# Performance work log

Hardware: AMD Instinct MI355X
Metric: run time of the kernel (lower is better)

The kernel has to match this reference:

```python
import jax, jax.numpy as jnp
import numpy as np
import math

NUM_HEADS = 8
DIM = 512
HEAD_DIM = DIM // NUM_HEADS
SCALE = HEAD_DIM ** -0.5
RP = 2            # remove_pad = kernel_size//2 * 2 for kernel_size=3
EPS_GN = 1e-5     # GroupNorm eps
EPS_L1 = 1e-12    # F.normalize eps


def _conv(x, w, b):
    # x: [B, Cin, H, W], w: [Cout, Cin, 3, 3] (OIHW), VALID padding, stride 1
    y = jax.lax.conv_general_dilated(x, w, (1, 1), 'VALID',
                                     dimension_numbers=('NCHW', 'OIHW', 'NCHW'))
    return y + b[None, :, None, None]


def _gn_per_channel(x, g, b):
    # GroupNorm with num_groups == num_channels: per-channel norm over (H, W)
    mu = x.mean(axis=(-2, -1), keepdims=True)
    var = x.var(axis=(-2, -1), keepdims=True)
    xn = (x - mu) * jax.lax.rsqrt(var + EPS_GN)
    return xn * g[None, :, None, None] + b[None, :, None, None]


def _ppe(rpe, c1w, c1b, g1w, g1b, c2w, c2b, g2w, g2b):
    # PeripheralPositionEncoding: rpe [side^2, side^2, 4*H] -> [1, H, N, N], N=(side-2*RP)^2
    nr, _, d = rpe.shape
    side = int(round(math.sqrt(nr)))
    s2 = side - 2 * RP
    x = rpe.reshape(side, side, side, side, d)          # i j k l d
    x = x[RP:side - RP, RP:side - RP]                   # trim i, j borders
    x = x.transpose(0, 1, 4, 2, 3).reshape(s2 * s2, d, side, side)  # (ij) d k l
    x = jax.nn.relu(_gn_per_channel(_conv(x, c1w, c1b), g1w, g1b))
    x = _gn_per_channel(_conv(x, c2w, c2b), g2w, g2b)   # [(ij), H, s2, s2]
    y = x.reshape(s2 * s2, NUM_HEADS, s2 * s2).transpose(1, 0, 2)[None]  # [1,H,N,N]
    return jax.nn.sigmoid(y)


def setup_inputs() -> dict:
    key = jax.random.key(0)
    ks = jax.random.split(key, 12)
    B, N = 8, 1024            # N = (36 - 4)^2
    side = 36
    cin = NUM_HEADS * 4       # 32
    inp = {
        'x': jax.random.normal(ks[0], (B, N, DIM), jnp.float32),
        'rpe_embed': jax.random.normal(ks[1], (side * side, side * side, cin), jnp.float32),
        'wqkv': jax.random.normal(ks[2], (3 * DIM, DIM), jnp.float32) * 0.02,
        'wproj': jax.random.normal(ks[3], (DIM, DIM), jnp.float32) * 0.02,
        'bproj': jnp.zeros((DIM,), jnp.float32),
        'c1w': jax.random.normal(ks[4], (cin, cin, 3, 3), jnp.float32) * 0.02,
        'c1b': jnp.zeros((cin,), jnp.float32),
        'g1w': jnp.ones((cin,), jnp.float32),
        'g1b': jnp.zeros((cin,), jnp.float32),
        'c2w': jax.random.normal(ks[5], (NUM_HEADS, cin, 3, 3), jnp.float32) * 0.02,
        'c2b': jnp.zeros((NUM_HEADS,), jnp.float32),
        'g2w': jnp.ones((NUM_HEADS,), jnp.float32),        # norm_init[1] = 1.0
        'g2b': jnp.zeros((NUM_HEADS,), jnp.float32),       # norm_init[0] = 0.0
    }
    return inp


def reference(x, rpe_embed, wqkv, wproj, bproj, c1w, c1b, g1w, g1b, c2w, c2b, g2w, g2b):
    B, N, D = x.shape
    H, HD = NUM_HEADS, HEAD_DIM
    qkv = x @ wqkv.T                                   # [B, N, 3D]
    q, k, v = jnp.split(qkv, 3, axis=-1)
    def heads(t):
        return t.reshape(B, N, H, HD).transpose(0, 2, 1, 3)  # [B, H, N, HD]
    q, k, v = heads(q), heads(k), heads(v)
    dots = jnp.einsum('bhnd,bhmd->bhnm', q, k) * SCALE
    dots = jnp.exp(dots - dots.max(axis=-1, keepdims=True))  # stable exp-score
    w = _ppe(rpe_embed, c1w, c1b, g1w, g1b, c2w, c2b, g2w, g2b)  # [1,H,N,N]
    attn = w * dots
    attn = attn / jnp.maximum(jnp.abs(attn).sum(axis=-1, keepdims=True), EPS_L1)  # L1 normalize
    out = jnp.einsum('bhnm,bhmd->bhnd', attn, v)
    out = out.transpose(0, 2, 1, 3).reshape(B, N, D)
    return out @ wproj.T + bproj
```

## Files before the change

### kernel.cpp

```cpp
#include <hip/hip_runtime.h>
#include <hip/hip_fp16.h>


typedef __attribute__((ext_vector_type(8))) short bf16x8;
typedef __attribute__((ext_vector_type(8))) _Float16 f16x8;
typedef __attribute__((ext_vector_type(4))) float f32x4;

__device__ __forceinline__ unsigned short f2bf(float f) {
  unsigned u = __builtin_bit_cast(unsigned, f);
  u += 0x7FFFu + ((u >> 16) & 1u);
  return (unsigned short)(u >> 16);
}

template<bool OUT_BF16>
__global__ __launch_bounds__(256) void gemm_f16_bt(
    const float* __restrict__ A, const float* __restrict__ B,
    void* __restrict__ Cv, const float* __restrict__ bias,
    int M, int N, int K)
{
  __shared__ __align__(16) _Float16 As[128 * 40];
  __shared__ __align__(16) _Float16 Bs[128 * 40];
  const int tid = threadIdx.x;
  const int wv = tid >> 6, ln = tid & 63, lr = ln & 15, lq = ln >> 4;
  const int wm = wv >> 1, wn = wv & 1;
  const int m0 = blockIdx.y * 128, n0 = blockIdx.x * 128;

  f32x4 acc[4][4];
#pragma unroll
  for (int i = 0; i < 4; i++)
#pragma unroll
    for (int j = 0; j < 4; j++) acc[i][j] = (f32x4){0.f, 0.f, 0.f, 0.f};

  const int sr = tid >> 1, sk = (tid & 1) * 16;
  const float* Ap = A + (size_t)(m0 + sr) * K + sk;
  const float* Bp = B + (size_t)(n0 + sr) * K + sk;

  for (int k0 = 0; k0 < K; k0 += 32) {
    float4 av0 = *(const float4*)(Ap + k0);
    float4 av1 = *(const float4*)(Ap + k0 + 4);
    float4 av2 = *(const float4*)(Ap + k0 + 8);
    float4 av3 = *(const float4*)(Ap + k0 + 12);
    float4 bv0 = *(const float4*)(Bp + k0);
    float4 bv1 = *(const float4*)(Bp + k0 + 4);
    float4 bv2 = *(const float4*)(Bp + k0 + 8);
    float4 bv3 = *(const float4*)(Bp + k0 + 12);
    __syncthreads();
    {
      f16x8 p0, p1, r0, r1;
      p0[0]=(_Float16)av0.x; p0[1]=(_Float16)av0.y; p0[2]=(_Float16)av0.z; p0[3]=(_Float16)av0.w;
      p0[4]=(_Float16)av1.x; p0[5]=(_Float16)av1.y; p0[6]=(_Float16)av1.z; p0[7]=(_Float16)av1.w;
      p1[0]=(_Float16)av2.x; p1[1]=(_Float16)av2.y; p1[2]=(_Float16)av2.z; p1[3]=(_Float16)av2.w;
      p1[4]=(_Float16)av3.x; p1[5]=(_Float16)av3.y; p1[6]=(_Float16)av3.z; p1[7]=(_Float16)av3.w;
      r0[0]=(_Float16)bv0.x; r0[1]=(_Float16)bv0.y; r0[2]=(_Float16)bv0.z; r0[3]=(_Float16)bv0.w;
      r0[4]=(_Float16)bv1.x; r0[5]=(_Float16)bv1.y; r0[6]=(_Float16)bv1.z; r0[7]=(_Float16)bv1.w;
      r1[0]=(_Float16)bv2.x; r1[1]=(_Float16)bv2.y; r1[2]=(_Float16)bv2.z; r1[3]=(_Float16)bv2.w;
      r1[4]=(_Float16)bv3.x; r1[5]=(_Float16)bv3.y; r1[6]=(_Float16)bv3.z; r1[7]=(_Float16)bv3.w;
      *(f16x8*)&As[sr * 40 + sk] = p0;
      *(f16x8*)&As[sr * 40 + sk + 8] = p1;
      *(f16x8*)&Bs[sr * 40 + sk] = r0;
      *(f16x8*)&Bs[sr * 40 + sk + 8] = r1;
    }
    __syncthreads();
    f16x8 af[4], bf[4];
#pragma unroll
    for (int mf = 0; mf < 4; mf++)
      af[mf] = *(const f16x8*)&As[(wm * 64 + mf * 16 + lr) * 40 + lq * 8];
#pragma unroll
    for (int nf = 0; nf < 4; nf++)
      bf[nf] = *(const f16x8*)&Bs[(wn * 64 + nf * 16 + lr) * 40 + lq * 8];
#pragma unroll
    for (int mf = 0; mf < 4; mf++)
#pragma unroll
      for (int nf = 0; nf < 4; nf++)
        acc[mf][nf] = __builtin_amdgcn_mfma_f32_16x16x32_f16(af[mf], bf[nf], acc[mf][nf], 0, 0, 0);
  }

#pragma unroll
  for (int mf = 0; mf < 4; mf++)
#pragma unroll
    for (int reg = 0; reg < 4; reg++) {
      const int row = m0 + wm * 64 + mf * 16 + lq * 4 + reg;
#pragma unroll
      for (int nf = 0; nf < 4; nf++) {
        const int col = n0 + wn * 64 + nf * 16 + lr;
        float v = acc[mf][nf][reg];
        if (bias) v += bias[col];
        if (OUT_BF16) ((unsigned short*)Cv)[(size_t)row * N + col] = f2bf(v);
        else          ((float*)Cv)[(size_t)row * N + col] = v;
      }
    }
}

__global__ __launch_bounds__(1024, 1) void conv_fused(
    const float* __restrict__ rpe,
    const float* __restrict__ c1w, const float* __restrict__ g1, const float* __restrict__ b1,
    const float* __restrict__ c2w, const float* __restrict__ g2, const float* __restrict__ b2,
    float* __restrict__ wout)
{
  extern __shared__ __align__(16) char smem[];
  unsigned short* inA = (unsigned short*)smem;
  unsigned short* yB  = (unsigned short*)(smem + 82944);
  unsigned short* wH1 = yB;
  unsigned short* wH2 = (unsigned short*)(smem + 156928);
  float* statA = (float*)(smem + 162688);
  float* aL    = (float*)(smem + 162944);
  float* cL    = aL + 32;
  float* transF = (float*)smem;

  const int tid = threadIdx.x;
  const int wv = tid >> 6, ln = tid & 63;
  const int lr = ln & 15, lq = ln >> 4;
  const int p = blockIdx.x;

  if (tid < 64) statA[tid] = 0.f;

  const float* src = rpe + (size_t)(((p >> 5) + 2) * 36 + (p & 31) + 2) * 41472;
  for (int t = tid; t < 10368; t += 1024) {
    int pix = t >> 3, dq = (t & 7) << 2;
    float4 v = *(const float4*)(src + pix * 32 + dq);
    __half2 h0 = __floats2half2_rn(v.x, v.y);
    __half2 h1 = __floats2half2_rn(v.z, v.w);
    uint2 u; u.x = __builtin_bit_cast(unsigned, h0); u.y = __builtin_bit_cast(unsigned, h1);
    *(uint2*)&inA[(dq >> 3) * 10368 + pix * 8 + (dq & 7)] = u;
  }
  for (int t = tid; t < 9216; t += 1024) {
    int oc = t / 288, rem = t - oc * 288;
    int ic = rem / 9, tap = rem - ic * 9;
    wH1[(tap * 32 + (oc & 1) * 16 + (oc >> 1)) * 40 + ic] = __half_as_ushort(__float2half(c1w[t]));
  }
  for (int t = tid; t < 2304; t += 1024) {
    int oc = t / 288, rem = t - oc * 288;
    int ic = rem / 9, tap = rem - ic * 9;
    wH2[(tap * 8 + oc) * 40 + ic] = __half_as_ushort(__float2half(c2w[t]));
  }
  __syncthreads();

  f16x8 w1f[2][9];
  const int ic0 = lq * 8;
#pragma unroll
  for (int ct = 0; ct < 2; ct++)
#pragma unroll
    for (int tap = 0; tap < 9; tap++)
      w1f[ct][tap] = *(const f16x8*)&wH1[(tap * 32 + ct * 16 + lr) * 40 + ic0];
  __syncthreads();

  constexpr int OFF1[9] = {0, 8, 16, 288, 296, 304, 576, 584, 592};
  float s0 = 0.f, q0 = 0.f, s1 = 0.f, q1 = 0.f;
  const unsigned short* inAg = inA + lq * 10368;
  for (int t = wv; t < 73; t += 16) {
    int m = t * 16 + lr;
    int ms = m < 1155 ? m : 1155;
    const unsigned short* ab = inAg + ((ms / 34) * 36 + (ms % 34)) * 8;
    f32x4 c0 = {0.f, 0.f, 0.f, 0.f}, c1v = {0.f, 0.f, 0.f, 0.f};
#pragma unroll
    for (int tap = 0; tap < 9; tap++) {
      f16x8 av = *(const f16x8*)(ab + OFF1[tap]);
      c0  = __builtin_amdgcn_mfma_f32_16x16x32_f16(av, w1f[0][tap], c0, 0, 0, 0);
      c1v = __builtin_amdgcn_mfma_f32_16x16x32_f16(av, w1f[1][tap], c1v, 0, 0, 0);
    }
#pragma unroll
    for (int r = 0; r < 4; r++) {
      int mo = t * 16 + lq * 4 + r;
      if (mo < 1156) {
        float v0 = c0[r], v1 = c1v[r];
        unsigned u = (unsigned)__half_as_ushort(__float2half(v0))
                   | ((unsigned)__half_as_ushort(__float2half(v1)) << 16);
        *(unsigned*)&yB[(lr >> 2) * 9248 + mo * 8 + ((lr * 2) & 7)] = u;
        s0 += v0; q0 += v0 * v0; s1 += v1; q1 += v1 * v1;
      }
    }
  }
#pragma unroll
  for (int off = 16; off < 64; off <<= 1) {
    s0 += __shfl_xor(s0, off); q0 += __shfl_xor(q0, off);
    s1 += __shfl_xor(s1, off); q1 += __shfl_xor(q1, off);
  }
  if (ln < 16) {
    atomicAdd(&statA[ln], s0);      atomicAdd(&statA[16 + ln], q0);
    atomicAdd(&statA[32 + ln], s1); atomicAdd(&statA[48 + ln], q1);
  }
  __syncthreads();
  if (tid < 32) {
    int cti = tid >> 4, lri = tid & 15;
    float s = statA[cti * 32 + lri];
    float q = statA[cti * 32 + 16 + lri];
    int ch = 2 * lri + cti;
    float mu = s * (1.f / 1156.f);
    float var = q * (1.f / 1156.f) - mu * mu;
    float a_ = rsqrtf(var + 1e-5f) * g1[ch];
    aL[ch] = a_; cL[ch] = b1[ch] - mu * a_;
  }
  if (tid < 16) statA[tid] = 0.f;
  __syncthreads();

  {
    int g = tid >> 8, ocb = g * 8;
    unsigned short* yg = yB + g * 9248;
    for (int pix = (tid & 255); pix < 1156; pix += 256) {
      f16x8 raw = *(const f16x8*)&yg[pix * 8];
      f16x8 outv;
#pragma unroll
      for (int e = 0; e < 8; e++) {
        float v = (float)raw[e];
        v = fmaxf(v * aL[ocb + e] + cL[ocb + e], 0.f);
        outv[e] = (_Float16)v;
      }
      *(f16x8*)&yg[pix * 8] = outv;
    }
  }
  __syncthreads();

  f16x8 w2f[9];
#pragma unroll
  for (int tap = 0; tap < 9; tap++)
    w2f[tap] = *(const f16x8*)&wH2[(tap * 8 + (lr & 7)) * 40 + ic0];

  constexpr int OFF2[9] = {0, 8, 16, 272, 280, 288, 544, 552, 560};
  const unsigned short* yBg = yB + lq * 9248;
  float s2 = 0.f, q2 = 0.f;
  for (int t = wv; t < 64; t += 16) {
    int m = t * 16 + lr;
    const unsigned short* ab = yBg + ((m >> 5) * 34 + (m & 31)) * 8;
    f32x4 cc = {0.f, 0.f, 0.f, 0.f};
#pragma unroll
    for (int tap = 0; tap < 9; tap++) {
      f16x8 av = *(const f16x8*)(ab + OFF2[tap]);
      cc = __builtin_amdgcn_mfma_f32_16x16x32_f16(av, w2f[tap], cc, 0, 0, 0);
    }
#pragma unroll
    for (int r = 0; r < 4; r++) {
      int mo = t * 16 + lq * 4 + r;
      float v = cc[r];
      if (lr < 8) {
        s2 += v; q2 += v * v;
        transF[lr * 1032 + mo] = v;
      }
    }
  }
#pragma unroll
  for (int off = 16; off < 64; off <<= 1) {
    s2 += __shfl_xor(s2, off); q2 += __shfl_xor(q2, off);
  }
  if (ln < 8) { atomicAdd(&statA[ln], s2); atomicAdd(&statA[8 + ln], q2); }
  __syncthreads();
  if (tid < 8) {
    float s = statA[tid], q = statA[8 + tid];
    float mu = s * (1.f / 1024.f);
    float var = q * (1.f / 1024.f) - mu * mu;
    float a_ = rsqrtf(var + 1e-5f) * g2[tid];
    aL[tid] = a_; cL[tid] = b2[tid] - mu * a_;
  }
  __syncthreads();

  for (int idx = tid; idx < 2048; idx += 1024) {
    int oc = idx >> 8, p4 = (idx & 255) << 2;
    float4 v = *(const float4*)&transF[oc * 1032 + p4];
    float a_ = aL[oc], c_ = cL[oc];
    float4 o;
    o.x = 1.f / (1.f + __expf(-(v.x * a_ + c_)));
    o.y = 1.f / (1.f + __expf(-(v.y * a_ + c_)));
    o.z = 1.f / (1.f + __expf(-(v.z * a_ + c_)));
    o.w = 1.f / (1.f + __expf(-(v.w * a_ + c_)));
    *(float4*)(wout + ((size_t)oc << 20) + ((size_t)p << 10) + p4) = o;
  }
}

__global__ __launch_bounds__(256) void attn_kernel(
    const unsigned short* __restrict__ qkv,
    const float* __restrict__ wppe,
    float* __restrict__ oh)
{
  __shared__ __align__(16) unsigned short k_lds[64 * 72];
  __shared__ __align__(16) unsigned short v_lds[64 * 72];
  __shared__ __align__(16) unsigned short p_lds[4 * 16 * 72];
  const int tid = threadIdx.x;
  const int wv = tid >> 6, ln = tid & 63;
  const int lr = ln & 15, lq = ln >> 4;
  const int b = blockIdx.y >> 3, h = blockIdx.y & 7;
  const int n0 = blockIdx.x << 6;

  const size_t qoff = (size_t)((b << 10) + n0 + (wv << 4) + lr) * 1536 + (h << 6);
  bf16x8 qf0 = *(const bf16x8*)(qkv + qoff + lq * 8);
  bf16x8 qf1 = *(const bf16x8*)(qkv + qoff + 32 + lq * 8);

  f32x4 acc[4];
#pragma unroll
  for (int dt = 0; dt < 4; dt++) acc[dt] = (f32x4){0.f, 0.f, 0.f, 0.f};
  float den[4] = {0.f, 0.f, 0.f, 0.f};
  const float* wp = wppe + ((size_t)h << 20);

  for (int m0 = 0; m0 < 1024; m0 += 64) {
    __syncthreads();
    for (int t = tid; t < 512; t += 256) {
      int m = t >> 3, dq = t & 7;
      const unsigned short* kr = qkv + (size_t)((b << 10) + m0 + m) * 1536 + 512 + (h << 6) + dq * 8;
      *(uint4*)&k_lds[m * 72 + dq * 8] = *(const uint4*)kr;
      uint4 vvv = *(const uint4*)(kr + 512);
      unsigned short tmp[8];
      *(uint4*)tmp = vvv;
#pragma unroll
      for (int i = 0; i < 8; i++) {
        int d = dq * 8 + i;
        v_lds[d * 72 + (m ^ (((d >> 3) & 7) << 3))] = tmp[i];
      }
    }
    __syncthreads();

    f32x4 s[4];
#pragma unroll
    for (int mt = 0; mt < 4; mt++) {
      const unsigned short* kb = &k_lds[(mt * 16 + lr) * 72 + lq * 8];
      f32x4 cz = (f32x4){0.f, 0.f, 0.f, 0.f};
      cz = __builtin_amdgcn_mfma_f32_16x16x32_bf16(qf0, *(const bf16x8*)kb, cz, 0, 0, 0);
      cz = __builtin_amdgcn_mfma_f32_16x16x32_bf16(qf1, *(const bf16x8*)(kb + 32), cz, 0, 0, 0);
      s[mt] = cz;
    }
#pragma unroll
    for (int mt = 0; mt < 4; mt++)
#pragma unroll
      for (int reg = 0; reg < 4; reg++) {
        int rrow = lq * 4 + reg;
        float wvl = wp[(size_t)(n0 + (wv << 4) + rrow) * 1024 + (m0 + mt * 16 + lr)];
        float pv = wvl * __expf(s[mt][reg] * 0.125f);
        den[reg] += pv;
        p_lds[((wv << 4) + rrow) * 72 + mt * 16 + lr] = f2bf(pv);
      }
    const unsigned short* pb = &p_lds[((wv << 4) + lr) * 72];
    bf16x8 pa0 = *(const bf16x8*)(pb + lq * 8);
    bf16x8 pa1 = *(const bf16x8*)(pb + 32 + lq * 8);
#pragma unroll
    for (int dt = 0; dt < 4; dt++) {
      int d = dt * 16 + lr;
      int sw = ((d >> 3) & 7) << 3;
      const unsigned short* vb = &v_lds[d * 72];
      acc[dt] = __builtin_amdgcn_mfma_f32_16x16x32_bf16(pa0, *(const bf16x8*)(vb + ((lq * 8) ^ sw)), acc[dt], 0, 0, 0);
      acc[dt] = __builtin_amdgcn_mfma_f32_16x16x32_bf16(pa1, *(const bf16x8*)(vb + ((32 + lq * 8) ^ sw)), acc[dt], 0, 0, 0);
    }
  }
#pragma unroll
  for (int off = 1; off < 16; off <<= 1)
#pragma unroll
    for (int reg = 0; reg < 4; reg++) den[reg] += __shfl_xor(den[reg], off);
#pragma unroll
  for (int dt = 0; dt < 4; dt++)
#pragma unroll
    for (int reg = 0; reg < 4; reg++) {
      size_t row = (size_t)((b << 10) + n0 + (wv << 4) + lq * 4 + reg);
      oh[row * 512 + (h << 6) + dt * 16 + lr] = acc[dt][reg] / den[reg];
    }
}

extern "C" void kernel_launch(void* const* d_in, const int* in_sizes, int n_in,
                              void* d_out, int out_size, void* d_ws, size_t ws_size,
                              hipStream_t stream) {
  (void)in_sizes; (void)n_in; (void)out_size; (void)ws_size;
  const float* x     = (const float*)d_in[0];
  const float* rpe   = (const float*)d_in[1];
  const float* wqkv  = (const float*)d_in[2];
  const float* wproj = (const float*)d_in[3];
  const float* bproj = (const float*)d_in[4];
  const float* c1w   = (const float*)d_in[5];
  const float* g1w   = (const float*)d_in[7];
  const float* g1b   = (const float*)d_in[8];
  const float* c2w   = (const float*)d_in[9];
  const float* g2w   = (const float*)d_in[11];
  const float* g2b   = (const float*)d_in[12];
  float* out = (float*)d_out;

  char* ws = (char*)d_ws;
  unsigned short* qkv_bf = (unsigned short*)ws;
  float* wppe = (float*)(ws + 25165824);
  float* ohb  = (float*)(ws + 58720256);

  gemm_f16_bt<true><<<dim3(12, 64), 256, 0, stream>>>(x, wqkv, qkv_bf, nullptr, 8192, 1536, 512);

  const int ldsC = 163200;
  hipFuncSetAttribute(reinterpret_cast<const void*>(&conv_fused),
                      hipFuncAttributeMaxDynamicSharedMemorySize, ldsC);
  conv_fused<<<1024, 1024, ldsC, stream>>>(rpe, c1w, g1w, g1b, c2w, g2w, g2b, wppe);

  attn_kernel<<<dim3(16, 64), 256, 0, stream>>>(qkv_bf, wppe, ohb);

  gemm_f16_bt<false><<<dim3(4, 64), 256, 0, stream>>>(ohb, wproj, out, bproj, 8192, 512, 512);
}
```

Baseline: 209.2 us.

## Split fused conv into two kernels with smaller LDS for higher occupancy

Replaces the single 1024-thread conv kernel, which used about 163KB of LDS and so fit one block per CU, with two kernels. conv1_k computes conv1 on half-images in 512-thread blocks with about 67KB of LDS and writes fp16 intermediates to global workspace. conv2_k reloads them, computes the GroupNorm statistics in a separate pass, then runs conv2 with its results kept in registers. The aim is more concurrent blocks per CU, so latency is hidden better, at the cost of an extra global round-trip for the intermediate and an additional launch. The y1g buffer reuses the ohb workspace region, which is safe because the writes are stream-ordered.

```diff
diff --git a/kernel.cpp b/kernel.cpp
--- a/kernel.cpp
+++ b/kernel.cpp
@@ -91,19 +91,81 @@
     }
 }
 
-__global__ __launch_bounds__(1024, 1) void conv_fused(
-    const float* __restrict__ rpe,
-    const float* __restrict__ c1w, const float* __restrict__ g1, const float* __restrict__ b1,
-    const float* __restrict__ c2w, const float* __restrict__ g2, const float* __restrict__ b2,
+__global__ __launch_bounds__(512, 4) void conv1_k(
+    const float* __restrict__ rpe, const float* __restrict__ c1w,
+    unsigned short* __restrict__ y1g)
+{
+  extern __shared__ __align__(16) char smem[];
+  unsigned short* inH = (unsigned short*)smem;
+  unsigned short* wH1 = (unsigned short*)(smem + 43776);
+
+  const int tid = threadIdx.x;
+  const int wv = tid >> 6, ln = tid & 63;
+  const int lr = ln & 15, lq = ln >> 4;
+  const int img = blockIdx.x >> 1, h = blockIdx.x & 1;
+
+  const float* src = rpe + (size_t)(((img >> 5) + 2) * 36 + (img & 31) + 2) * 41472
+                   + h * 19584;
+  for (int t = tid; t < 5472; t += 512) {
+    int pix = t >> 3, dq = (t & 7) << 2;
+    float4 v = *(const float4*)(src + t * 4);
+    __half2 h0 = __floats2half2_rn(v.x, v.y);
+    __half2 h1 = __floats2half2_rn(v.z, v.w);
+    uint2 u; u.x = __builtin_bit_cast(unsigned, h0); u.y = __builtin_bit_cast(unsigned, h1);
+    *(uint2*)&inH[(dq >> 3) * 5472 + pix * 8 + (dq & 7)] = u;
+  }
+  for (int t = tid; t < 9216; t += 512) {
+    int oc = t / 288, rem = t - oc * 288;
+    int ic = rem / 9, tap = rem - ic * 9;
+    wH1[(tap * 32 + (oc & 1) * 16 + (oc >> 1)) * 40 + ic] = __half_as_ushort(__float2half(c1w[t]));
+  }
+  __syncthreads();
+
+  const int ic0 = lq * 8;
+  f16x8 w1f[2][9];
+#pragma unroll
+  for (int ct = 0; ct < 2; ct++)
+#pragma unroll
+    for (int tap = 0; tap < 9; tap++)
+      w1f[ct][tap] = *(const f16x8*)&wH1[(tap * 32 + ct * 16 + lr) * 40 + ic0];
+
+  constexpr int OFF1[9] = {0, 8, 16, 288, 296, 304, 576, 584, 592};
+  unsigned short* ybase = y1g + (size_t)img * 36992 + (lr >> 2) * 9248 + ((2 * lr) & 7);
+  const unsigned short* inAg = inH + lq * 5472;
+  for (int t = wv; t < 37; t += 8) {
+    int m = t * 16 + lr;
+    int ms = m < 577 ? m : 577;
+    const unsigned short* ab = inAg + ((ms / 34) * 36 + (ms % 34)) * 8;
+    f32x4 c0 = {0.f, 0.f, 0.f, 0.f}, c1v = {0.f, 0.f, 0.f, 0.f};
+#pragma unroll
+    for (int tap = 0; tap < 9; tap++) {
+      f16x8 av = *(const f16x8*)(ab + OFF1[tap]);
+      c0  = __builtin_amdgcn_mfma_f32_16x16x32_f16(av, w1f[0][tap], c0, 0, 0, 0);
+      c1v = __builtin_amdgcn_mfma_f32_16x16x32_f16(av, w1f[1][tap], c1v, 0, 0, 0);
+    }
+#pragma unroll
+    for (int r = 0; r < 4; r++) {
+      int mo = t * 16 + lq * 4 + r;
+      if (mo < 578) {
+        unsigned u = (unsigned)__half_as_ushort(__float2half(c0[r]))
+                   | ((unsigned)__half_as_ushort(__float2half(c1v[r])) << 16);
+        *(unsigned*)(ybase + (h * 578 + mo) * 8) = u;
+      }
+    }
+  }
+}
+
+__global__ __launch_bounds__(512, 4) void conv2_k(
+    const unsigned short* __restrict__ y1g, const float* __restrict__ c2w,
+    const float* __restrict__ g1, const float* __restrict__ b1,
+    const float* __restrict__ g2, const float* __restrict__ b2,
     float* __restrict__ wout)
 {
   extern __shared__ __align__(16) char smem[];
-  unsigned short* inA = (unsigned short*)smem;
-  unsigned short* yB  = (unsigned short*)(smem + 82944);
-  unsigned short* wH1 = yB;
-  unsigned short* wH2 = (unsigned short*)(smem + 156928);
-  float* statA = (float*)(smem + 162688);
-  float* aL    = (float*)(smem + 162944);
+  unsigned short* yB  = (unsigned short*)smem;
+  unsigned short* wH2 = (unsigned short*)(smem + 73984);
+  float* statA = (float*)(smem + 79744);
+  float* aL    = statA + 64;
   float* cL    = aL + 32;
   float* transF = (float*)smem;
 
@@ -114,111 +176,85 @@
 
   if (tid < 64) statA[tid] = 0.f;
 
-  const float* src = rpe + (size_t)(((p >> 5) + 2) * 36 + (p & 31) + 2) * 41472;
-  for (int t = tid; t < 10368; t += 1024) {
-    int pix = t >> 3, dq = (t & 7) << 2;
-    float4 v = *(const float4*)(src + pix * 32 + dq);
-    __half2 h0 = __floats2half2_rn(v.x, v.y);
-    __half2 h1 = __floats2half2_rn(v.z, v.w);
-    uint2 u; u.x = __builtin_bit_cast(unsigned, h0); u.y = __builtin_bit_cast(unsigned, h1);
-    *(uint2*)&inA[(dq >> 3) * 10368 + pix * 8 + (dq & 7)] = u;
-  }
-  for (int t = tid; t < 9216; t += 1024) {
-    int oc = t / 288, rem = t - oc * 288;
-    int ic = rem / 9, tap = rem - ic * 9;
-    wH1[(tap * 32 + (oc & 1) * 16 + (oc >> 1)) * 40 + ic] = __half_as_ushort(__float2half(c1w[t]));
-  }
-  for (int t = tid; t < 2304; t += 1024) {
+  const unsigned short* src = y1g + (size_t)p * 36992;
+  for (int t = tid; t < 4624; t += 512)
+    *(uint4*)&yB[t * 8] = *(const uint4*)(src + t * 8);
+  for (int t = tid; t < 2304; t += 512) {
     int oc = t / 288, rem = t - oc * 288;
     int ic = rem / 9, tap = rem - ic * 9;
     wH2[(tap * 8 + oc) * 40 + ic] = __half_as_ushort(__float2half(c2w[t]));
   }
   __syncthreads();
 
-  f16x8 w1f[2][9];
-  const int ic0 = lq * 8;
-#pragma unroll
-  for (int ct = 0; ct < 2; ct++)
-#pragma unroll
-    for (int tap = 0; tap < 9; tap++)
-      w1f[ct][tap] = *(const f16x8*)&wH1[(tap * 32 + ct * 16 + lr) * 40 + ic0];
-  __syncthreads();
-
-  constexpr int OFF1[9] = {0, 8, 16, 288, 296, 304, 576, 584, 592};
-  float s0 = 0.f, q0 = 0.f, s1 = 0.f, q1 = 0.f;
-  const unsigned short* inAg = inA + lq * 10368;
-  for (int t = wv; t < 73; t += 16) {
-    int m = t * 16 + lr;
-    int ms = m < 1155 ? m : 1155;
-    const unsigned short* ab = inAg + ((ms / 34) * 36 + (ms % 34)) * 8;
-    f32x4 c0 = {0.f, 0.f, 0.f, 0.f}, c1v = {0.f, 0.f, 0.f, 0.f};
-#pragma unroll
-    for (int tap = 0; tap < 9; tap++) {
-      f16x8 av = *(const f16x8*)(ab + OFF1[tap]);
-      c0  = __builtin_amdgcn_mfma_f32_16x16x32_f16(av, w1f[0][tap], c0, 0, 0, 0);
-      c1v = __builtin_amdgcn_mfma_f32_16x16x32_f16(av, w1f[1][tap], c1v, 0, 0, 0);
-    }
-#pragma unroll
-    for (int r = 0; r < 4; r++) {
-      int mo = t * 16 + lq * 4 + r;
-      if (mo < 1156) {
-        float v0 = c0[r], v1 = c1v[r];
-        unsigned u = (unsigned)__half_as_ushort(__float2half(v0))
-                   | ((unsigned)__half_as_ushort(__float2half(v1)) << 16);
-        *(unsigned*)&yB[(lr >> 2) * 9248 + mo * 8 + ((lr * 2) & 7)] = u;
-        s0 += v0; q0 += v0 * v0; s1 += v1; q1 += v1 * v1;
-      }
-    }
-  }
-#pragma unroll
-  for (int off = 16; off < 64; off <<= 1) {
-    s0 += __shfl_xor(s0, off); q0 += __shfl_xor(q0, off);
-    s1 += __shfl_xor(s1, off); q1 += __shfl_xor(q1, off);
-  }
-  if (ln < 16) {
-    atomicAdd(&statA[ln], s0);      atomicAdd(&statA[16 + ln], q0);
-    atomicAdd(&statA[32 + ln], s1); atomicAdd(&statA[48 + ln], q1);
+  {
+    int g = wv >> 1;
+    float s[8], q[8];
+#pragma unroll
+    for (int e = 0; e < 8; e++) { s[e] = 0.f; q[e] = 0.f; }
+    int base = (wv & 1) * 64 + ln;
+    for (int k = 0; k < 10; k++) {
+      int pix = base + 128 * k;
+      if (pix < 1156) {
+        f16x8 v = *(const f16x8*)&yB[g * 9248 + pix * 8];
+#pragma unroll
+        for (int e = 0; e < 8; e++) { float f = (float)v[e]; s[e] += f; q[e] += f * f; }
+      }
+    }
+#pragma unroll
+    for (int off = 1; off < 64; off <<= 1)
+#pragma unroll
+      for (int e = 0; e < 8; e++) { s[e] += __shfl_xor(s[e], off); q[e] += __shfl_xor(q[e], off); }
+    if (ln == 0) {
+#pragma unroll
+      for (int e = 0; e < 8; e++) {
+        atomicAdd(&statA[g * 8 + e], s[e]);
+        atomicAdd(&statA[32 + g * 8 + e], q[e]);
+      }
+    }
   }
   __syncthreads();
   if (tid < 32) {
-    int cti = tid >> 4, lri = tid & 15;
-    float s = statA[cti * 32 + lri];
-    float q = statA[cti * 32 + 16 + lri];
-    int ch = 2 * lri + cti;
+    float s = statA[tid], q = statA[32 + tid];
     float mu = s * (1.f / 1156.f);
     float var = q * (1.f / 1156.f) - mu * mu;
-    float a_ = rsqrtf(var + 1e-5f) * g1[ch];
-    aL[ch] = a_; cL[ch] = b1[ch] - mu * a_;
+    float a_ = rsqrtf(var + 1e-5f) * g1[tid];
+    aL[tid] = a_; cL[tid] = b1[tid] - mu * a_;
   }
   if (tid < 16) statA[tid] = 0.f;
   __syncthreads();
 
   {
-    int g = tid >> 8, ocb = g * 8;
+    int g = tid >> 7, base = tid & 127;
     unsigned short* yg = yB + g * 9248;
-    for (int pix = (tid & 255); pix < 1156; pix += 256) {
-      f16x8 raw = *(const f16x8*)&yg[pix * 8];
-      f16x8 outv;
-#pragma unroll
-      for (int e = 0; e < 8; e++) {
-        float v = (float)raw[e];
-        v = fmaxf(v * aL[ocb + e] + cL[ocb + e], 0.f);
-        outv[e] = (_Float16)v;
-      }
-      *(f16x8*)&yg[pix * 8] = outv;
+    for (int k = 0; k < 10; k++) {
+      int pix = base + 128 * k;
+      if (pix < 1156) {
+        f16x8 raw = *(const f16x8*)&yg[pix * 8];
+        f16x8 outv;
+#pragma unroll
+        for (int e = 0; e < 8; e++) {
+          float v = (float)raw[e];
+          outv[e] = (_Float16)fmaxf(v * aL[g * 8 + e] + cL[g * 8 + e], 0.f);
+        }
+        *(f16x8*)&yg[pix * 8] = outv;
+      }
     }
   }
   __syncthreads();
 
   f16x8 w2f[9];
+  const int ic0 = lq * 8;
 #pragma unroll
   for (int tap = 0; tap < 9; tap++)
     w2f[tap] = *(const f16x8*)&wH2[(tap * 8 + (lr & 7)) * 40 + ic0];
 
   constexpr int OFF2[9] = {0, 8, 16, 272, 280, 288, 544, 552, 560};
   const unsigned short* yBg = yB + lq * 9248;
+  f32x4 zsave[8];
   float s2 = 0.f, q2 = 0.f;
-  for (int t = wv; t < 64; t += 16) {
+#pragma unroll
+  for (int i = 0; i < 8; i++) {
+    int t = wv + i * 8;
     int m = t * 16 + lr;
     const unsigned short* ab = yBg + ((m >> 5) * 34 + (m & 31)) * 8;
     f32x4 cc = {0.f, 0.f, 0.f, 0.f};
@@ -227,15 +263,9 @@
       f16x8 av = *(const f16x8*)(ab + OFF2[tap]);
       cc = __builtin_amdgcn_mfma_f32_16x16x32_f16(av, w2f[tap], cc, 0, 0, 0);
     }
-#pragma unroll
-    for (int r = 0; r < 4; r++) {
-      int mo = t * 16 + lq * 4 + r;
-      float v = cc[r];
-      if (lr < 8) {
-        s2 += v; q2 += v * v;
-        transF[lr * 1032 + mo] = v;
-      }
-    }
+    zsave[i] = cc;
+#pragma unroll
+    for (int r = 0; r < 4; r++) { s2 += cc[r]; q2 += cc[r] * cc[r]; }
   }
 #pragma unroll
   for (int off = 16; off < 64; off <<= 1) {
@@ -243,6 +273,16 @@
   }
   if (ln < 8) { atomicAdd(&statA[ln], s2); atomicAdd(&statA[8 + ln], q2); }
   __syncthreads();
+
+  if (lr < 8) {
+#pragma unroll
+    for (int i = 0; i < 8; i++) {
+      int t = wv + i * 8;
+#pragma unroll
+      for (int r = 0; r < 4; r++)
+        transF[lr * 1032 + t * 16 + lq * 4 + r] = zsave[i][r];
+    }
+  }
   if (tid < 8) {
     float s = statA[tid], q = statA[8 + tid];
     float mu = s * (1.f / 1024.f);
@@ -252,7 +292,7 @@
   }
   __syncthreads();
 
-  for (int idx = tid; idx < 2048; idx += 1024) {
+  for (int idx = tid; idx < 2048; idx += 512) {
     int oc = idx >> 8, p4 = (idx & 255) << 2;
     float4 v = *(const float4*)&transF[oc * 1032 + p4];
     float a_ = aL[oc], c_ = cL[oc];
@@ -370,14 +410,20 @@
   char* ws = (char*)d_ws;
   unsigned short* qkv_bf = (unsigned short*)ws;
   float* wppe = (float*)(ws + 25165824);
+  unsigned short* y1g = (unsigned short*)(ws + 58720256);
   float* ohb  = (float*)(ws + 58720256);
 
   gemm_f16_bt<true><<<dim3(12, 64), 256, 0, stream>>>(x, wqkv, qkv_bf, nullptr, 8192, 1536, 512);
 
-  const int ldsC = 163200;
-  hipFuncSetAttribute(reinterpret_cast<const void*>(&conv_fused),
-                      hipFuncAttributeMaxDynamicSharedMemorySize, ldsC);
-  conv_fused<<<1024, 1024, ldsC, stream>>>(rpe, c1w, g1w, g1b, c2w, g2w, g2b, wppe);
+  const int lds1 = 66816;
+  hipFuncSetAttribute(reinterpret_cast<const void*>(&conv1_k),
+                      hipFuncAttributeMaxDynamicSharedMemorySize, lds1);
+  conv1_k<<<2048, 512, lds1, stream>>>(rpe, c1w, y1g);
+
+  const int lds2 = 80256;
+  hipFuncSetAttribute(reinterpret_cast<const void*>(&conv2_k),
+                      hipFuncAttributeMaxDynamicSharedMemorySize, lds2);
+  conv2_k<<<1024, 512, lds2, stream>>>(y1g, c2w, g1w, g1b, g2w, g2b, wppe);
 
   attn_kernel<<<dim3(16, 64), 256, 0, stream>>>(qkv_bf, wppe, ohb);
 
```

Result: slower. 236.9 us (+13.2%).

## Read conv input directly from global and halve LDS to fit two blocks per CU

Applied to the files above, without the earlier changes.

The fused PPE conv kernel stops staging the full fp32 rpe patch into LDS as fp16. Instead each wave loads its conv1 input taps straight from global memory and converts them in registers. This cuts LDS use roughly in half and shrinks blocks to 512 threads, so more blocks can be resident per CU to overlap memory latency. Conv2 results are kept in registers until after the stats barrier so the transpose buffer can alias the conv1 output buffer. The cost is redundant global/L2 reads of overlapping 3x3 taps and higher register pressure.

```diff
diff --git a/kernel.cpp b/kernel.cpp
--- a/kernel.cpp
+++ b/kernel.cpp
@@ -91,20 +91,19 @@
     }
 }
 
-__global__ __launch_bounds__(1024, 1) void conv_fused(
+__global__ __launch_bounds__(512, 4) void conv_fused2(
     const float* __restrict__ rpe,
     const float* __restrict__ c1w, const float* __restrict__ g1, const float* __restrict__ b1,
     const float* __restrict__ c2w, const float* __restrict__ g2, const float* __restrict__ b2,
     float* __restrict__ wout)
 {
   extern __shared__ __align__(16) char smem[];
-  unsigned short* inA = (unsigned short*)smem;
-  unsigned short* yB  = (unsigned short*)(smem + 82944);
+  unsigned short* yB  = (unsigned short*)smem;
   unsigned short* wH1 = yB;
-  unsigned short* wH2 = (unsigned short*)(smem + 156928);
-  float* statA = (float*)(smem + 162688);
-  float* aL    = (float*)(smem + 162944);
-  float* cL    = aL + 32;
+  unsigned short* wH2 = (unsigned short*)(smem + 73984);
+  float* statA = (float*)(smem + 79744);
+  float* aL    = (float*)(smem + 80000);
+  float* cL    = (float*)(smem + 80128);
   float* transF = (float*)smem;
 
   const int tid = threadIdx.x;
@@ -114,21 +113,12 @@
 
   if (tid < 64) statA[tid] = 0.f;
 
-  const float* src = rpe + (size_t)(((p >> 5) + 2) * 36 + (p & 31) + 2) * 41472;
-  for (int t = tid; t < 10368; t += 1024) {
-    int pix = t >> 3, dq = (t & 7) << 2;
-    float4 v = *(const float4*)(src + pix * 32 + dq);
-    __half2 h0 = __floats2half2_rn(v.x, v.y);
-    __half2 h1 = __floats2half2_rn(v.z, v.w);
-    uint2 u; u.x = __builtin_bit_cast(unsigned, h0); u.y = __builtin_bit_cast(unsigned, h1);
-    *(uint2*)&inA[(dq >> 3) * 10368 + pix * 8 + (dq & 7)] = u;
-  }
-  for (int t = tid; t < 9216; t += 1024) {
+  for (int t = tid; t < 9216; t += 512) {
     int oc = t / 288, rem = t - oc * 288;
     int ic = rem / 9, tap = rem - ic * 9;
     wH1[(tap * 32 + (oc & 1) * 16 + (oc >> 1)) * 40 + ic] = __half_as_ushort(__float2half(c1w[t]));
   }
-  for (int t = tid; t < 2304; t += 1024) {
+  for (int t = tid; t < 2304; t += 512) {
     int oc = t / 288, rem = t - oc * 288;
     int ic = rem / 9, tap = rem - ic * 9;
     wH2[(tap * 8 + oc) * 40 + ic] = __half_as_ushort(__float2half(c2w[t]));
@@ -144,17 +134,21 @@
       w1f[ct][tap] = *(const f16x8*)&wH1[(tap * 32 + ct * 16 + lr) * 40 + ic0];
   __syncthreads();
 
-  constexpr int OFF1[9] = {0, 8, 16, 288, 296, 304, 576, 584, 592};
+  const float* src = rpe + (size_t)(((p >> 5) + 2) * 36 + (p & 31) + 2) * 41472;
+  constexpr int TOFF[9] = {0, 32, 64, 1152, 1184, 1216, 2304, 2336, 2368};
   float s0 = 0.f, q0 = 0.f, s1 = 0.f, q1 = 0.f;
-  const unsigned short* inAg = inA + lq * 10368;
-  for (int t = wv; t < 73; t += 16) {
+  for (int t = wv; t < 73; t += 8) {
     int m = t * 16 + lr;
     int ms = m < 1155 ? m : 1155;
-    const unsigned short* ab = inAg + ((ms / 34) * 36 + (ms % 34)) * 8;
+    const float* ab = src + ((ms / 34) * 36 + (ms % 34)) * 32 + lq * 8;
     f32x4 c0 = {0.f, 0.f, 0.f, 0.f}, c1v = {0.f, 0.f, 0.f, 0.f};
 #pragma unroll
     for (int tap = 0; tap < 9; tap++) {
-      f16x8 av = *(const f16x8*)(ab + OFF1[tap]);
+      float4 a0 = *(const float4*)(ab + TOFF[tap]);
+      float4 a1 = *(const float4*)(ab + TOFF[tap] + 4);
+      f16x8 av;
+      av[0]=(_Float16)a0.x; av[1]=(_Float16)a0.y; av[2]=(_Float16)a0.z; av[3]=(_Float16)a0.w;
+      av[4]=(_Float16)a1.x; av[5]=(_Float16)a1.y; av[6]=(_Float16)a1.z; av[7]=(_Float16)a1.w;
       c0  = __builtin_amdgcn_mfma_f32_16x16x32_f16(av, w1f[0][tap], c0, 0, 0, 0);
       c1v = __builtin_amdgcn_mfma_f32_16x16x32_f16(av, w1f[1][tap], c1v, 0, 0, 0);
     }
@@ -194,18 +188,20 @@
   __syncthreads();
 
   {
-    int g = tid >> 8, ocb = g * 8;
+    int g = tid >> 7, base = tid & 127;
     unsigned short* yg = yB + g * 9248;
-    for (int pix = (tid & 255); pix < 1156; pix += 256) {
-      f16x8 raw = *(const f16x8*)&yg[pix * 8];
-      f16x8 outv;
-#pragma unroll
-      for (int e = 0; e < 8; e++) {
-        float v = (float)raw[e];
-        v = fmaxf(v * aL[ocb + e] + cL[ocb + e], 0.f);
-        outv[e] = (_Float16)v;
-      }
-      *(f16x8*)&yg[pix * 8] = outv;
+    for (int k = 0; k < 10; k++) {
+      int pix = base + 128 * k;
+      if (pix < 1156) {
+        f16x8 raw = *(const f16x8*)&yg[pix * 8];
+        f16x8 outv;
+#pragma unroll
+        for (int e = 0; e < 8; e++) {
+          float v = (float)raw[e];
+          outv[e] = (_Float16)fmaxf(v * aL[g * 8 + e] + cL[g * 8 + e], 0.f);
+        }
+        *(f16x8*)&yg[pix * 8] = outv;
+      }
     }
   }
   __syncthreads();
@@ -217,8 +213,11 @@
 
   constexpr int OFF2[9] = {0, 8, 16, 272, 280, 288, 544, 552, 560};
   const unsigned short* yBg = yB + lq * 9248;
+  f32x4 zsave[8];
   float s2 = 0.f, q2 = 0.f;
-  for (int t = wv; t < 64; t += 16) {
+#pragma unroll
+  for (int i = 0; i < 8; i++) {
+    int t = wv + i * 8;
     int m = t * 16 + lr;
     const unsigned short* ab = yBg + ((m >> 5) * 34 + (m & 31)) * 8;
     f32x4 cc = {0.f, 0.f, 0.f, 0.f};
@@ -227,15 +226,9 @@
       f16x8 av = *(const f16x8*)(ab + OFF2[tap]);
       cc = __builtin_amdgcn_mfma_f32_16x16x32_f16(av, w2f[tap], cc, 0, 0, 0);
     }
-#pragma unroll
-    for (int r = 0; r < 4; r++) {
-      int mo = t * 16 + lq * 4 + r;
-      float v = cc[r];
-      if (lr < 8) {
-        s2 += v; q2 += v * v;
-        transF[lr * 1032 + mo] = v;
-      }
-    }
+    zsave[i] = cc;
+#pragma unroll
+    for (int r = 0; r < 4; r++) { s2 += cc[r]; q2 += cc[r] * cc[r]; }
   }
 #pragma unroll
   for (int off = 16; off < 64; off <<= 1) {
@@ -243,6 +236,16 @@
   }
   if (ln < 8) { atomicAdd(&statA[ln], s2); atomicAdd(&statA[8 + ln], q2); }
   __syncthreads();
+
+  if (lr < 8) {
+#pragma unroll
+    for (int i = 0; i < 8; i++) {
+      int t = wv + i * 8;
+#pragma unroll
+      for (int r = 0; r < 4; r++)
+        transF[lr * 1032 + t * 16 + lq * 4 + r] = zsave[i][r];
+    }
+  }
   if (tid < 8) {
     float s = statA[tid], q = statA[8 + tid];
     float mu = s * (1.f / 1024.f);
@@ -252,7 +255,7 @@
   }
   __syncthreads();
 
-  for (int idx = tid; idx < 2048; idx += 1024) {
+  for (int idx = tid; idx < 2048; idx += 512) {
     int oc = idx >> 8, p4 = (idx & 255) << 2;
     float4 v = *(const float4*)&transF[oc * 1032 + p4];
     float a_ = aL[oc], c_ = cL[oc];
@@ -374,10 +377,10 @@
 
   gemm_f16_bt<true><<<dim3(12, 64), 256, 0, stream>>>(x, wqkv, qkv_bf, nullptr, 8192, 1536, 512);
 
-  const int ldsC = 163200;
-  hipFuncSetAttribute(reinterpret_cast<const void*>(&conv_fused),
+  const int ldsC = 80256;
+  hipFuncSetAttribute(reinterpret_cast<const void*>(&conv_fused2),
                       hipFuncAttributeMaxDynamicSharedMemorySize, ldsC);
-  conv_fused<<<1024, 1024, ldsC, stream>>>(rpe, c1w, g1w, g1b, c2w, g2w, g2b, wppe);
+  conv_fused2<<<1024, 512, ldsC, stream>>>(rpe, c1w, g1w, g1b, c2w, g2w, g2b, wppe);
 
   attn_kernel<<<dim3(16, 64), 256, 0, stream>>>(qkv_bf, wppe, ohb);
 
```

Result: slower. 302.8 us (+44.7%).
